# Performance work log

Measured on AMD Instinct MI355X. Metric: run time of the kernel, lower is better.

Reference implementation:

```python
import jax, jax.numpy as jnp
import numpy as np

B = 32768
N_TABLES = 26
N_ROWS = 200000
D = 64
N_DENSE = 13
NUM_PAIRS = (N_TABLES + 1) * N_TABLES // 2  # 351, pairs j < i over 27 vectors


def setup_inputs() -> dict:
    key = jax.random.key(0)
    ks = jax.random.split(key, 16)
    def lin(kw, kb, m, n):
        W = jax.random.normal(kw, (m, n), jnp.float32) * np.sqrt(2.0 / (m + n))
        b = jax.random.normal(kb, (m,), jnp.float32) * np.sqrt(1.0 / m)
        return W, b
    bw0, bb0 = lin(ks[0], ks[1], 512, N_DENSE)
    bw1, bb1 = lin(ks[2], ks[3], 256, 512)
    bw2, bb2 = lin(ks[4], ks[5], D, 256)
    tw0, tb0 = lin(ks[6], ks[7], 512, D + NUM_PAIRS)
    tw1, tb1 = lin(ks[8], ks[9], 256, 512)
    tw2, tb2 = lin(ks[10], ks[11], 1, 256)
    bound = np.sqrt(1.0 / N_ROWS)
    emb_tables = jax.random.uniform(ks[12], (N_TABLES, N_ROWS, D), jnp.float32,
                                    minval=-bound, maxval=bound)
    dense_x = jax.random.uniform(ks[13], (B, N_DENSE), jnp.float32)
    indices = jax.random.randint(ks[14], (N_TABLES, B), 0, N_ROWS, jnp.int64)
    return {"dense_x": dense_x, "indices": indices, "emb_tables": emb_tables,
            "bw0": bw0, "bb0": bb0, "bw1": bw1, "bb1": bb1, "bw2": bw2, "bb2": bb2,
            "tw0": tw0, "tb0": tb0, "tw1": tw1, "tb1": tb1, "tw2": tw2, "tb2": tb2}


def reference(dense_x, indices, emb_tables,
              bw0, bb0, bw1, bb1, bw2, bb2,
              tw0, tb0, tw1, tb1, tw2, tb2):
    # bottom MLP (all ReLU, sigmoid_bot = -1)
    h = jax.nn.relu(dense_x @ bw0.T + bb0)
    h = jax.nn.relu(h @ bw1.T + bb1)
    x_bot = jax.nn.relu(h @ bw2.T + bb2)          # [B, D]

    # multi-table EmbeddingBag(sum) with single-index bags -> plain gather
    embs = jax.vmap(lambda tbl, idx: tbl[idx])(emb_tables, indices)  # [26, B, D]

    # dot interaction over 27 feature vectors
    T = jnp.concatenate([x_bot[None], embs], axis=0).transpose(1, 0, 2)  # [B, 27, D]
    Z = jnp.einsum('bnd,bmd->bnm', T, T)                                 # [B, 27, 27]
    li, lj = jnp.tril_indices(N_TABLES + 1, k=-1)  # pairs with j < i (no self)
    Zflat = Z[:, li, lj]                           # [B, 351]
    R = jnp.concatenate([x_bot, Zflat], axis=1)    # [B, 415]

    # top MLP: ReLU, ReLU, Sigmoid (sigmoid_top = 2)
    h = jax.nn.relu(R @ tw0.T + tb0)
    h = jax.nn.relu(h @ tw1.T + tb1)
    p = jax.nn.sigmoid(h @ tw2.T + tb2)            # [B, 1]
    return p
```

## Files before the change

kernel.cpp:

```cpp
#include <hip/hip_runtime.h>
#include <cstddef>
#include <cstdint>

#define B_SZ    32768
#define NTAB    26
#define NROWS   200000

typedef __attribute__((ext_vector_type(8))) short short8v;
typedef __attribute__((ext_vector_type(4))) float f32x4;
typedef __attribute__((ext_vector_type(16))) float f32x16;

__device__ __forceinline__ ushort f2bf(float f) {
    uint32_t u = __builtin_bit_cast(uint32_t, f);
    u += 0x7FFFu + ((u >> 16) & 1u);
    return (ushort)(u >> 16);
}
__device__ __forceinline__ float bf2f(ushort h) {
    uint32_t u = ((uint32_t)h) << 16;
    return __builtin_bit_cast(float, u);
}
__device__ __forceinline__ void stage16(const ushort* g, ushort* l) {
    __builtin_amdgcn_global_load_lds(
        (const __attribute__((address_space(1))) unsigned int*)g,
        (__attribute__((address_space(3))) unsigned int*)l, 16, 0, 0);
}

__global__ __launch_bounds__(256) void conv_all_k(
    const float* __restrict__ dense_x, const float* __restrict__ bw0,
    const float* __restrict__ tw0, const float* __restrict__ bw1,
    const float* __restrict__ bw2, const float* __restrict__ tw1,
    ushort* __restrict__ dense_pad, ushort* __restrict__ bw0p,
    ushort* __restrict__ tw0p, ushort* __restrict__ bw1c,
    ushort* __restrict__ bw2c, ushort* __restrict__ tw1c)
{
    const int gid = blockIdx.x * 256 + threadIdx.x;
    if (gid < 1048576) {
        int r = gid >> 5, k = gid & 31;
        dense_pad[gid] = (k < 13) ? f2bf(dense_x[r * 13 + k]) : (ushort)0;
    } else if (gid < 1064960) {
        int i = gid - 1048576; int r = i >> 5, k = i & 31;
        bw0p[i] = (k < 13) ? f2bf(bw0[r * 13 + k]) : (ushort)0;
    } else if (gid < 1277952) {
        int i = gid - 1064960; int r = i / 416, k = i - r * 416;
        tw0p[i] = (k < 415) ? f2bf(tw0[r * 415 + k]) : (ushort)0;
    } else if (gid < 1409024) {
        int i = gid - 1277952; bw1c[i] = f2bf(bw1[i]);
    } else if (gid < 1425408) {
        int i = gid - 1409024; bw2c[i] = f2bf(bw2[i]);
    } else if (gid < 1556480) {
        int i = gid - 1425408; tw1c[i] = f2bf(tw1[i]);
    }
}

__global__ __launch_bounds__(256, 2) void bot012_k(
    const ushort* __restrict__ dense_pad, const ushort* __restrict__ bw0p,
    const float* __restrict__ bb0, const ushort* __restrict__ bw1c,
    const float* __restrict__ bb1, const ushort* __restrict__ bw2c,
    const float* __restrict__ bb2, ushort* __restrict__ Rb)
{
    __shared__ __align__(16) ushort h0s[32 * 512];
    __shared__ __align__(16) ushort Wst[2][256 * 32];
    __shared__ __align__(16) ushort h1s[32 * 256];
    const int t = threadIdx.x;
    const int lane = t & 63, w = t >> 6;
    const int fr = lane & 15, j16 = lane >> 4;
    const int bBase = blockIdx.x * 32;

    if (t < 128) {
        const int r = t >> 2, u = t & 3, us = u ^ ((r >> 1) & 3);
        stage16(dense_pad + (size_t)(bBase + r) * 32 + us * 8, &h1s[t * 8]);
    }
#pragma unroll
    for (int i = 0; i < 4; ++i) {
        const int idx = i * 256 + t;
        const int r = idx >> 2, u = idx & 3, us = u ^ ((r >> 1) & 3);
        stage16(bw0p + (size_t)r * 32 + us * 8, &Wst[0][idx * 8]);
        stage16(bw0p + (size_t)(256 + r) * 32 + us * 8, &Wst[1][idx * 8]);
    }
    __syncthreads();

    f32x4 acc0[2][2][4] = {};
    {
        short8v a[2];
#pragma unroll
        for (int m = 0; m < 2; ++m) {
            const int r = m * 16 + fr;
            a[m] = *(const short8v*)&h1s[r * 32 + (j16 ^ ((r >> 1) & 3)) * 8];
        }
#pragma unroll
        for (int hh = 0; hh < 2; ++hh) {
            short8v b[4];
#pragma unroll
            for (int n = 0; n < 4; ++n) {
                const int lr = w * 64 + n * 16 + fr;
                b[n] = *(const short8v*)&Wst[hh][lr * 32 + (j16 ^ ((lr >> 1) & 3)) * 8];
            }
            __builtin_amdgcn_s_setprio(1);
#pragma unroll
            for (int m = 0; m < 2; ++m)
#pragma unroll
                for (int n = 0; n < 4; ++n)
                    acc0[hh][m][n] = __builtin_amdgcn_mfma_f32_16x16x32_bf16(b[n], a[m], acc0[hh][m][n], 0, 0, 0);
            __builtin_amdgcn_s_setprio(0);
        }
    }
    __syncthreads();

#pragma unroll
    for (int i = 0; i < 4; ++i) {
        const int idx = i * 256 + t;
        const int r = idx >> 2, u = idx & 3, us = u ^ ((r >> 1) & 3);
        stage16(bw1c + (size_t)r * 512 + us * 8, &Wst[0][idx * 8]);
        stage16(bw1c + (size_t)r * 512 + 32 + us * 8, &Wst[1][idx * 8]);
    }
#pragma unroll
    for (int hh = 0; hh < 2; ++hh)
#pragma unroll
    for (int n = 0; n < 4; ++n) {
        const int ch = hh * 256 + w * 64 + n * 16 + j16 * 4;
        const float4 bv = *(const float4*)&bb0[ch];
#pragma unroll
        for (int m = 0; m < 2; ++m) {
            const int s = m * 16 + fr;
            ushort4 o;
            o.x = f2bf(fmaxf(acc0[hh][m][n][0] + bv.x, 0.f));
            o.y = f2bf(fmaxf(acc0[hh][m][n][1] + bv.y, 0.f));
            o.z = f2bf(fmaxf(acc0[hh][m][n][2] + bv.z, 0.f));
            o.w = f2bf(fmaxf(acc0[hh][m][n][3] + bv.w, 0.f));
            const int u = ch >> 3, su = u ^ (s & 7);
            *(ushort4*)&h0s[s * 512 + su * 8 + (ch & 7)] = o;
        }
    }
    __syncthreads();

    f32x4 acc1[2][4] = {};
    for (int i8 = 0; i8 < 8; ++i8) {
        const int ktA = i8 * 64, ktB = ktA + 32;
#pragma unroll
        for (int half = 0; half < 2; ++half) {
            const int kt = half ? ktB : ktA;
            short8v a[2], b[4];
#pragma unroll
            for (int m = 0; m < 2; ++m) {
                const int s = m * 16 + fr;
                const int u = (kt >> 3) + j16, su = u ^ (s & 7);
                a[m] = *(const short8v*)&h0s[s * 512 + su * 8];
            }
#pragma unroll
            for (int n = 0; n < 4; ++n) {
                const int lr = w * 64 + n * 16 + fr;
                b[n] = *(const short8v*)&Wst[half][lr * 32 + (j16 ^ ((lr >> 1) & 3)) * 8];
            }
            __builtin_amdgcn_s_setprio(1);
#pragma unroll
            for (int m = 0; m < 2; ++m)
#pragma unroll
                for (int n = 0; n < 4; ++n)
                    acc1[m][n] = __builtin_amdgcn_mfma_f32_16x16x32_bf16(b[n], a[m], acc1[m][n], 0, 0, 0);
            __builtin_amdgcn_s_setprio(0);
        }
        __syncthreads();
        if (i8 < 7) {
            const int kt2 = (i8 + 1) * 64;
#pragma unroll
            for (int i = 0; i < 4; ++i) {
                const int idx = i * 256 + t;
                const int r = idx >> 2, u = idx & 3, us = u ^ ((r >> 1) & 3);
                stage16(bw1c + (size_t)r * 512 + kt2 + us * 8, &Wst[0][idx * 8]);
                stage16(bw1c + (size_t)r * 512 + kt2 + 32 + us * 8, &Wst[1][idx * 8]);
            }
            __syncthreads();
        }
    }
    {
        const int r = t >> 2, u = t & 3, us = u ^ ((r >> 1) & 3);
        stage16(bw2c + (size_t)r * 256 + us * 8, &Wst[0][t * 8]);
        stage16(bw2c + (size_t)r * 256 + 32 + us * 8, &Wst[1][t * 8]);
    }
#pragma unroll
    for (int n = 0; n < 4; ++n) {
        const int ch = w * 64 + n * 16 + j16 * 4;
        const float4 bv = *(const float4*)&bb1[ch];
#pragma unroll
        for (int m = 0; m < 2; ++m) {
            const int s = m * 16 + fr;
            ushort4 o;
            o.x = f2bf(fmaxf(acc1[m][n][0] + bv.x, 0.f));
            o.y = f2bf(fmaxf(acc1[m][n][1] + bv.y, 0.f));
            o.z = f2bf(fmaxf(acc1[m][n][2] + bv.z, 0.f));
            o.w = f2bf(fmaxf(acc1[m][n][3] + bv.w, 0.f));
            const int u = ch >> 3, su = u ^ (s & 7);
            *(ushort4*)&h1s[s * 256 + su * 8 + (ch & 7)] = o;
        }
    }
    __syncthreads();

    f32x4 acc2[2] = {};
    for (int i8 = 0; i8 < 4; ++i8) {
#pragma unroll
        for (int half = 0; half < 2; ++half) {
            const int kt = i8 * 64 + half * 32;
            short8v a[2], b;
#pragma unroll
            for (int m = 0; m < 2; ++m) {
                const int s = m * 16 + fr;
                const int u = (kt >> 3) + j16, su = u ^ (s & 7);
                a[m] = *(const short8v*)&h1s[s * 256 + su * 8];
            }
            {
                const int lr = w * 16 + fr;
                b = *(const short8v*)&Wst[half][lr * 32 + (j16 ^ ((lr >> 1) & 3)) * 8];
            }
#pragma unroll
            for (int m = 0; m < 2; ++m)
                acc2[m] = __builtin_amdgcn_mfma_f32_16x16x32_bf16(b, a[m], acc2[m], 0, 0, 0);
        }
        __syncthreads();
        if (i8 < 3) {
            const int kt2 = (i8 + 1) * 64;
            const int r = t >> 2, u = t & 3, us = u ^ ((r >> 1) & 3);
            stage16(bw2c + (size_t)r * 256 + kt2 + us * 8, &Wst[0][t * 8]);
            stage16(bw2c + (size_t)r * 256 + kt2 + 32 + us * 8, &Wst[1][t * 8]);
            __syncthreads();
        }
    }
    {
        const int ch = w * 16 + j16 * 4;
        const float4 bv = *(const float4*)&bb2[ch];
#pragma unroll
        for (int m = 0; m < 2; ++m) {
            const int s = m * 16 + fr;
            ushort4 o;
            o.x = f2bf(fmaxf(acc2[m][0] + bv.x, 0.f));
            o.y = f2bf(fmaxf(acc2[m][1] + bv.y, 0.f));
            o.z = f2bf(fmaxf(acc2[m][2] + bv.z, 0.f));
            o.w = f2bf(fmaxf(acc2[m][3] + bv.w, 0.f));
            *(ushort4*)&Rb[(size_t)(bBase + s) * 64 + ch] = o;
        }
    }
}

__global__ __launch_bounds__(256, 2) void topint_k(
    const float* __restrict__ emb, const int* __restrict__ indices,
    const ushort* __restrict__ Rb, const ushort* __restrict__ tw0p,
    const float* __restrict__ tb0, const ushort* __restrict__ tw1c,
    const float* __restrict__ tb1, const float* __restrict__ tw2,
    const float* __restrict__ tb2, float* __restrict__ out)
{
    __shared__ __align__(16) ushort U[32 * 512];
    __shared__ __align__(16) ushort Wst[2][256 * 32];
    __shared__ __align__(16) int scratch[832];
    const int t = threadIdx.x;
    const int lane = t & 63, w = t >> 6;
    const int fr = lane & 15, j16 = lane >> 4;
    const int bBase = blockIdx.x * 32;

    {
        const int r = t >> 3, u = t & 7;
        short8v v = *(const short8v*)&Rb[(size_t)(bBase + r) * 64 + u * 8];
        *(short8v*)&U[r * 424 + u * 8] = v;
    }
    if (t < 32) U[t * 424 + 415] = 0;
    for (int e = t; e < 832; e += 256)
        scratch[e] = indices[(size_t)(e >> 5) * B_SZ + bBase + (e & 31)];
    __syncthreads();

#pragma unroll
    for (int i = 0; i < 4; ++i) {
        const int idx = i * 256 + t;
        const int r = idx >> 2, u = idx & 3, us = u ^ ((r >> 1) & 3);
        stage16(tw0p + (size_t)r * 416 + us * 8, &Wst[0][idx * 8]);
        stage16(tw0p + (size_t)(256 + r) * 416 + us * 8, &Wst[1][idx * 8]);
    }

    {
        const int r32 = lane & 31, half = lane >> 5;
        for (int it = 0; it < 8; ++it) {
            const int s = it * 4 + w;
            short8v tf[4];
            if (r32 == 0) {
#pragma unroll
                for (int kq = 0; kq < 4; ++kq)
                    tf[kq] = *(const short8v*)&U[s * 424 + kq * 16 + half * 8];
            } else if (r32 <= 26) {
                const int idxv = scratch[(r32 - 1) * 32 + s];
                const float* rp = emb + ((size_t)(r32 - 1) * NROWS + (size_t)idxv) * 64 + half * 8;
#pragma unroll
                for (int kq = 0; kq < 4; ++kq) {
                    const f32x4 x = *(const f32x4*)&rp[kq * 16];
                    const f32x4 y = *(const f32x4*)&rp[kq * 16 + 4];
                    short8v v;
                    v[0] = (short)f2bf(x[0]); v[1] = (short)f2bf(x[1]);
                    v[2] = (short)f2bf(x[2]); v[3] = (short)f2bf(x[3]);
                    v[4] = (short)f2bf(y[0]); v[5] = (short)f2bf(y[1]);
                    v[6] = (short)f2bf(y[2]); v[7] = (short)f2bf(y[3]);
                    tf[kq] = v;
                }
            } else {
#pragma unroll
                for (int kq = 0; kq < 4; ++kq) tf[kq] = (short8v)0;
            }
            f32x16 c = {};
#pragma unroll
            for (int kq = 0; kq < 4; ++kq)
                c = __builtin_amdgcn_mfma_f32_32x32x16_bf16(tf[kq], tf[kq], c, 0, 0, 0);
#pragma unroll
            for (int reg = 0; reg < 16; ++reg) {
                const int r = (reg & 3) + 8 * (reg >> 2) + 4 * half;
                if (r < 27 && r32 < r)
                    U[s * 424 + 64 + (r * (r - 1)) / 2 + r32] = f2bf(c[reg]);
            }
        }
    }
    __syncthreads();

    f32x4 accA[2][2][4] = {};
    for (int kt_i = 0; kt_i < 13; ++kt_i) {
        const int kt = kt_i * 32;
        short8v a[2];
#pragma unroll
        for (int m = 0; m < 2; ++m) {
            const int s = m * 16 + fr;
            a[m] = *(const short8v*)&U[s * 424 + ((kt >> 3) + j16) * 8];
        }
#pragma unroll
        for (int hh = 0; hh < 2; ++hh) {
            short8v b[4];
#pragma unroll
            for (int n = 0; n < 4; ++n) {
                const int lr = w * 64 + n * 16 + fr;
                b[n] = *(const short8v*)&Wst[hh][lr * 32 + (j16 ^ ((lr >> 1) & 3)) * 8];
            }
            __builtin_amdgcn_s_setprio(1);
#pragma unroll
            for (int m = 0; m < 2; ++m)
#pragma unroll
                for (int n = 0; n < 4; ++n)
                    accA[hh][m][n] = __builtin_amdgcn_mfma_f32_16x16x32_bf16(b[n], a[m], accA[hh][m][n], 0, 0, 0);
            __builtin_amdgcn_s_setprio(0);
        }
        __syncthreads();
        if (kt_i < 12) {
            const int kt2 = kt + 32;
#pragma unroll
            for (int i = 0; i < 4; ++i) {
                const int idx = i * 256 + t;
                const int r = idx >> 2, u = idx & 3, us = u ^ ((r >> 1) & 3);
                stage16(tw0p + (size_t)r * 416 + kt2 + us * 8, &Wst[0][idx * 8]);
                stage16(tw0p + (size_t)(256 + r) * 416 + kt2 + us * 8, &Wst[1][idx * 8]);
            }
            __syncthreads();
        }
    }
#pragma unroll
    for (int i = 0; i < 4; ++i) {
        const int idx = i * 256 + t;
        const int r = idx >> 2, u = idx & 3, us = u ^ ((r >> 1) & 3);
        stage16(tw1c + (size_t)r * 512 + us * 8, &Wst[0][idx * 8]);
        stage16(tw1c + (size_t)r * 512 + 32 + us * 8, &Wst[1][idx * 8]);
    }
#pragma unroll
    for (int hh = 0; hh < 2; ++hh)
#pragma unroll
    for (int n = 0; n < 4; ++n) {
        const int ch = hh * 256 + w * 64 + n * 16 + j16 * 4;
        const float4 bv = *(const float4*)&tb0[ch];
#pragma unroll
        for (int m = 0; m < 2; ++m) {
            const int s = m * 16 + fr;
            ushort4 o;
            o.x = f2bf(fmaxf(accA[hh][m][n][0] + bv.x, 0.f));
            o.y = f2bf(fmaxf(accA[hh][m][n][1] + bv.y, 0.f));
            o.z = f2bf(fmaxf(accA[hh][m][n][2] + bv.z, 0.f));
            o.w = f2bf(fmaxf(accA[hh][m][n][3] + bv.w, 0.f));
            const int u = ch >> 3, su = u ^ (s & 7);
            *(ushort4*)&U[s * 512 + su * 8 + (ch & 7)] = o;
        }
    }
    __syncthreads();

    f32x4 acc2[2][4] = {};
    for (int i8 = 0; i8 < 8; ++i8) {
#pragma unroll
        for (int half = 0; half < 2; ++half) {
            const int kt = i8 * 64 + half * 32;
            short8v a[2], b[4];
#pragma unroll
            for (int m = 0; m < 2; ++m) {
                const int s = m * 16 + fr;
                const int u = (kt >> 3) + j16, su = u ^ (s & 7);
                a[m] = *(const short8v*)&U[s * 512 + su * 8];
            }
#pragma unroll
            for (int n = 0; n < 4; ++n) {
                const int lr = w * 64 + n * 16 + fr;
                b[n] = *(const short8v*)&Wst[half][lr * 32 + (j16 ^ ((lr >> 1) & 3)) * 8];
            }
            __builtin_amdgcn_s_setprio(1);
#pragma unroll
            for (int m = 0; m < 2; ++m)
#pragma unroll
                for (int n = 0; n < 4; ++n)
                    acc2[m][n] = __builtin_amdgcn_mfma_f32_16x16x32_bf16(b[n], a[m], acc2[m][n], 0, 0, 0);
            __builtin_amdgcn_s_setprio(0);
        }
        __syncthreads();
        if (i8 < 7) {
            const int kt2 = (i8 + 1) * 64;
#pragma unroll
            for (int i = 0; i < 4; ++i) {
                const int idx = i * 256 + t;
                const int r = idx >> 2, u = idx & 3, us = u ^ ((r >> 1) & 3);
                stage16(tw1c + (size_t)r * 512 + kt2 + us * 8, &Wst[0][idx * 8]);
                stage16(tw1c + (size_t)r * 512 + kt2 + 32 + us * 8, &Wst[1][idx * 8]);
            }
            __syncthreads();
        }
    }

    float* red = (float*)scratch;
    float part[2] = {0.f, 0.f};
#pragma unroll
    for (int n = 0; n < 4; ++n) {
        const int ch = w * 64 + n * 16 + j16 * 4;
        const float4 bv = *(const float4*)&tb1[ch];
        const float4 wv = *(const float4*)&tw2[ch];
#pragma unroll
        for (int m = 0; m < 2; ++m) {
            part[m] += fmaxf(acc2[m][n][0] + bv.x, 0.f) * wv.x
                     + fmaxf(acc2[m][n][1] + bv.y, 0.f) * wv.y
                     + fmaxf(acc2[m][n][2] + bv.z, 0.f) * wv.z
                     + fmaxf(acc2[m][n][3] + bv.w, 0.f) * wv.w;
        }
    }
#pragma unroll
    for (int m = 0; m < 2; ++m) {
        float v = part[m];
        v += __shfl_xor(v, 16, 64);
        v += __shfl_xor(v, 32, 64);
        if (lane < 16) red[w * 32 + m * 16 + fr] = v;
    }
    __syncthreads();
    if (t < 32) {
        const float sm = red[t] + red[32 + t] + red[64 + t] + red[96 + t];
        out[bBase + t] = 1.f / (1.f + expf(-(sm + tb2[0])));
    }
}

extern "C" void kernel_launch(void* const* d_in, const int* in_sizes, int n_in,
                              void* d_out, int out_size, void* d_ws, size_t ws_size,
                              hipStream_t stream)
{
    (void)in_sizes; (void)n_in; (void)out_size; (void)ws_size;
    const float* dense_x = (const float*)d_in[0];
    const int*   indices = (const int*)d_in[1];
    const float* emb     = (const float*)d_in[2];
    const float* bw0 = (const float*)d_in[3];
    const float* bb0 = (const float*)d_in[4];
    const float* bw1 = (const float*)d_in[5];
    const float* bb1 = (const float*)d_in[6];
    const float* bw2 = (const float*)d_in[7];
    const float* bb2 = (const float*)d_in[8];
    const float* tw0 = (const float*)d_in[9];
    const float* tb0 = (const float*)d_in[10];
    const float* tw1 = (const float*)d_in[11];
    const float* tb1 = (const float*)d_in[12];
    const float* tw2 = (const float*)d_in[13];
    const float* tb2 = (const float*)d_in[14];
    float* out = (float*)d_out;

    ushort* ws16      = (ushort*)d_ws;
    ushort* dense_pad = ws16;
    ushort* Rb        = dense_pad + (size_t)B_SZ * 32;
    ushort* bw0p      = Rb + (size_t)B_SZ * 64;
    ushort* tw0p      = bw0p + 512 * 32;
    ushort* bw1c      = tw0p + 512 * 416;
    ushort* bw2c      = bw1c + 256 * 512;
    ushort* tw1c      = bw2c + 64 * 256;

    conv_all_k<<<dim3(6080), dim3(256), 0, stream>>>(
        dense_x, bw0, tw0, bw1, bw2, tw1,
        dense_pad, bw0p, tw0p, bw1c, bw2c, tw1c);

    bot012_k<<<dim3(B_SZ / 32), dim3(256), 0, stream>>>(
        dense_pad, bw0p, bb0, bw1c, bb1, bw2c, bb2, Rb);

    topint_k<<<dim3(B_SZ / 32), dim3(256), 0, stream>>>(
        emb, indices, Rb, tw0p, tb0, tw1c, tb1, tw2, tb2, out);
}
```

Measured before the change: 116.9 us.

## Fuse bottom MLP and interaction/top MLP into a single kernel

Merges the bottom-MLP kernel and the interaction+top-MLP kernel into one launch per 32-row tile. x_bot is written straight into the shared-memory R buffer instead of a global Rb round trip, and the shared buffers are reused across stages. The embedding indices are loaded into registers at kernel start so their latency overlaps with the bottom MLP. This removes one kernel launch and the global write/read of the intermediate, in exchange for longer register live ranges and a more complex single kernel.

```diff
diff --git a/kernel.cpp b/kernel.cpp
--- a/kernel.cpp
+++ b/kernel.cpp
@@ -14,10 +14,6 @@
     uint32_t u = __builtin_bit_cast(uint32_t, f);
     u += 0x7FFFu + ((u >> 16) & 1u);
     return (ushort)(u >> 16);
-}
-__device__ __forceinline__ float bf2f(ushort h) {
-    uint32_t u = ((uint32_t)h) << 16;
-    return __builtin_bit_cast(float, u);
 }
 __device__ __forceinline__ void stage16(const ushort* g, ushort* l) {
     __builtin_amdgcn_global_load_lds(
@@ -52,23 +48,34 @@
     }
 }
 
-__global__ __launch_bounds__(256, 2) void bot012_k(
+__global__ __launch_bounds__(256, 2) void fused_k(
     const ushort* __restrict__ dense_pad, const ushort* __restrict__ bw0p,
     const float* __restrict__ bb0, const ushort* __restrict__ bw1c,
     const float* __restrict__ bb1, const ushort* __restrict__ bw2c,
-    const float* __restrict__ bb2, ushort* __restrict__ Rb)
+    const float* __restrict__ bb2,
+    const float* __restrict__ emb, const int* __restrict__ indices,
+    const ushort* __restrict__ tw0p, const float* __restrict__ tb0,
+    const ushort* __restrict__ tw1c, const float* __restrict__ tb1,
+    const float* __restrict__ tw2, const float* __restrict__ tb2,
+    float* __restrict__ out)
 {
-    __shared__ __align__(16) ushort h0s[32 * 512];
+    __shared__ __align__(16) ushort R1[32 * 512];
     __shared__ __align__(16) ushort Wst[2][256 * 32];
-    __shared__ __align__(16) ushort h1s[32 * 256];
+    __shared__ __align__(16) ushort R3[32 * 256];
     const int t = threadIdx.x;
     const int lane = t & 63, w = t >> 6;
     const int fr = lane & 15, j16 = lane >> 4;
     const int bBase = blockIdx.x * 32;
 
+    int ir0, ir1, ir2, ir3;
+    ir0 = indices[(size_t)(t >> 5) * B_SZ + bBase + (t & 31)];
+    ir1 = indices[(size_t)((256 + t) >> 5) * B_SZ + bBase + ((256 + t) & 31)];
+    ir2 = indices[(size_t)((512 + t) >> 5) * B_SZ + bBase + ((512 + t) & 31)];
+    ir3 = (t < 64) ? indices[(size_t)((768 + t) >> 5) * B_SZ + bBase + ((768 + t) & 31)] : 0;
+
     if (t < 128) {
         const int r = t >> 2, u = t & 3, us = u ^ ((r >> 1) & 3);
-        stage16(dense_pad + (size_t)(bBase + r) * 32 + us * 8, &h1s[t * 8]);
+        stage16(dense_pad + (size_t)(bBase + r) * 32 + us * 8, &R3[t * 8]);
     }
 #pragma unroll
     for (int i = 0; i < 4; ++i) {
@@ -85,7 +92,7 @@
 #pragma unroll
         for (int m = 0; m < 2; ++m) {
             const int r = m * 16 + fr;
-            a[m] = *(const short8v*)&h1s[r * 32 + (j16 ^ ((r >> 1) & 3)) * 8];
+            a[m] = *(const short8v*)&R3[r * 32 + (j16 ^ ((r >> 1) & 3)) * 8];
         }
 #pragma unroll
         for (int hh = 0; hh < 2; ++hh) {
@@ -128,23 +135,22 @@
             o.z = f2bf(fmaxf(acc0[hh][m][n][2] + bv.z, 0.f));
             o.w = f2bf(fmaxf(acc0[hh][m][n][3] + bv.w, 0.f));
             const int u = ch >> 3, su = u ^ (s & 7);
-            *(ushort4*)&h0s[s * 512 + su * 8 + (ch & 7)] = o;
+            *(ushort4*)&R1[s * 512 + su * 8 + (ch & 7)] = o;
         }
     }
     __syncthreads();
 
     f32x4 acc1[2][4] = {};
     for (int i8 = 0; i8 < 8; ++i8) {
-        const int ktA = i8 * 64, ktB = ktA + 32;
 #pragma unroll
         for (int half = 0; half < 2; ++half) {
-            const int kt = half ? ktB : ktA;
+            const int kt = i8 * 64 + half * 32;
             short8v a[2], b[4];
 #pragma unroll
             for (int m = 0; m < 2; ++m) {
                 const int s = m * 16 + fr;
                 const int u = (kt >> 3) + j16, su = u ^ (s & 7);
-                a[m] = *(const short8v*)&h0s[s * 512 + su * 8];
+                a[m] = *(const short8v*)&R1[s * 512 + su * 8];
             }
 #pragma unroll
             for (int n = 0; n < 4; ++n) {
@@ -190,7 +196,7 @@
             o.z = f2bf(fmaxf(acc1[m][n][2] + bv.z, 0.f));
             o.w = f2bf(fmaxf(acc1[m][n][3] + bv.w, 0.f));
             const int u = ch >> 3, su = u ^ (s & 7);
-            *(ushort4*)&h1s[s * 256 + su * 8 + (ch & 7)] = o;
+            *(ushort4*)&R3[s * 256 + su * 8 + (ch & 7)] = o;
         }
     }
     __syncthreads();
@@ -205,7 +211,7 @@
             for (int m = 0; m < 2; ++m) {
                 const int s = m * 16 + fr;
                 const int u = (kt >> 3) + j16, su = u ^ (s & 7);
-                a[m] = *(const short8v*)&h1s[s * 256 + su * 8];
+                a[m] = *(const short8v*)&R3[s * 256 + su * 8];
             }
             {
                 const int lr = w * 16 + fr;
@@ -235,36 +241,15 @@
             o.y = f2bf(fmaxf(acc2[m][1] + bv.y, 0.f));
             o.z = f2bf(fmaxf(acc2[m][2] + bv.z, 0.f));
             o.w = f2bf(fmaxf(acc2[m][3] + bv.w, 0.f));
-            *(ushort4*)&Rb[(size_t)(bBase + s) * 64 + ch] = o;
-        }
-    }
-}
-
-__global__ __launch_bounds__(256, 2) void topint_k(
-    const float* __restrict__ emb, const int* __restrict__ indices,
-    const ushort* __restrict__ Rb, const ushort* __restrict__ tw0p,
-    const float* __restrict__ tb0, const ushort* __restrict__ tw1c,
-    const float* __restrict__ tb1, const float* __restrict__ tw2,
-    const float* __restrict__ tb2, float* __restrict__ out)
-{
-    __shared__ __align__(16) ushort U[32 * 512];
-    __shared__ __align__(16) ushort Wst[2][256 * 32];
-    __shared__ __align__(16) int scratch[832];
-    const int t = threadIdx.x;
-    const int lane = t & 63, w = t >> 6;
-    const int fr = lane & 15, j16 = lane >> 4;
-    const int bBase = blockIdx.x * 32;
-
+            *(ushort4*)&R1[s * 424 + ch] = o;
+        }
+    }
+    if (t < 32) R1[t * 424 + 415] = 0;
     {
-        const int r = t >> 3, u = t & 7;
-        short8v v = *(const short8v*)&Rb[(size_t)(bBase + r) * 64 + u * 8];
-        *(short8v*)&U[r * 424 + u * 8] = v;
-    }
-    if (t < 32) U[t * 424 + 415] = 0;
-    for (int e = t; e < 832; e += 256)
-        scratch[e] = indices[(size_t)(e >> 5) * B_SZ + bBase + (e & 31)];
-    __syncthreads();
-
+        int* sc = (int*)R3;
+        sc[t] = ir0; sc[256 + t] = ir1; sc[512 + t] = ir2;
+        if (t < 64) sc[768 + t] = ir3;
+    }
 #pragma unroll
     for (int i = 0; i < 4; ++i) {
         const int idx = i * 256 + t;
@@ -272,8 +257,10 @@
         stage16(tw0p + (size_t)r * 416 + us * 8, &Wst[0][idx * 8]);
         stage16(tw0p + (size_t)(256 + r) * 416 + us * 8, &Wst[1][idx * 8]);
     }
+    __syncthreads();
 
     {
+        const int* sc = (const int*)R3;
         const int r32 = lane & 31, half = lane >> 5;
         for (int it = 0; it < 8; ++it) {
             const int s = it * 4 + w;
@@ -281,9 +268,9 @@
             if (r32 == 0) {
 #pragma unroll
                 for (int kq = 0; kq < 4; ++kq)
-                    tf[kq] = *(const short8v*)&U[s * 424 + kq * 16 + half * 8];
+                    tf[kq] = *(const short8v*)&R1[s * 424 + kq * 16 + half * 8];
             } else if (r32 <= 26) {
-                const int idxv = scratch[(r32 - 1) * 32 + s];
+                const int idxv = sc[(r32 - 1) * 32 + s];
                 const float* rp = emb + ((size_t)(r32 - 1) * NROWS + (size_t)idxv) * 64 + half * 8;
 #pragma unroll
                 for (int kq = 0; kq < 4; ++kq) {
@@ -308,7 +295,7 @@
             for (int reg = 0; reg < 16; ++reg) {
                 const int r = (reg & 3) + 8 * (reg >> 2) + 4 * half;
                 if (r < 27 && r32 < r)
-                    U[s * 424 + 64 + (r * (r - 1)) / 2 + r32] = f2bf(c[reg]);
+                    R1[s * 424 + 64 + (r * (r - 1)) / 2 + r32] = f2bf(c[reg]);
             }
         }
     }
@@ -321,7 +308,7 @@
 #pragma unroll
         for (int m = 0; m < 2; ++m) {
             const int s = m * 16 + fr;
-            a[m] = *(const short8v*)&U[s * 424 + ((kt >> 3) + j16) * 8];
+            a[m] = *(const short8v*)&R1[s * 424 + ((kt >> 3) + j16) * 8];
         }
 #pragma unroll
         for (int hh = 0; hh < 2; ++hh) {
@@ -374,12 +361,12 @@
             o.z = f2bf(fmaxf(accA[hh][m][n][2] + bv.z, 0.f));
             o.w = f2bf(fmaxf(accA[hh][m][n][3] + bv.w, 0.f));
             const int u = ch >> 3, su = u ^ (s & 7);
-            *(ushort4*)&U[s * 512 + su * 8 + (ch & 7)] = o;
-        }
-    }
-    __syncthreads();
-
-    f32x4 acc2[2][4] = {};
+            *(ushort4*)&R1[s * 512 + su * 8 + (ch & 7)] = o;
+        }
+    }
+    __syncthreads();
+
+    f32x4 accB[2][4] = {};
     for (int i8 = 0; i8 < 8; ++i8) {
 #pragma unroll
         for (int half = 0; half < 2; ++half) {
@@ -389,7 +376,7 @@
             for (int m = 0; m < 2; ++m) {
                 const int s = m * 16 + fr;
                 const int u = (kt >> 3) + j16, su = u ^ (s & 7);
-                a[m] = *(const short8v*)&U[s * 512 + su * 8];
+                a[m] = *(const short8v*)&R1[s * 512 + su * 8];
             }
 #pragma unroll
             for (int n = 0; n < 4; ++n) {
@@ -401,7 +388,7 @@
             for (int m = 0; m < 2; ++m)
 #pragma unroll
                 for (int n = 0; n < 4; ++n)
-                    acc2[m][n] = __builtin_amdgcn_mfma_f32_16x16x32_bf16(b[n], a[m], acc2[m][n], 0, 0, 0);
+                    accB[m][n] = __builtin_amdgcn_mfma_f32_16x16x32_bf16(b[n], a[m], accB[m][n], 0, 0, 0);
             __builtin_amdgcn_s_setprio(0);
         }
         __syncthreads();
@@ -418,7 +405,7 @@
         }
     }
 
-    float* red = (float*)scratch;
+    float* red = (float*)R3;
     float part[2] = {0.f, 0.f};
 #pragma unroll
     for (int n = 0; n < 4; ++n) {
@@ -427,10 +414,10 @@
         const float4 wv = *(const float4*)&tw2[ch];
 #pragma unroll
         for (int m = 0; m < 2; ++m) {
-            part[m] += fmaxf(acc2[m][n][0] + bv.x, 0.f) * wv.x
-                     + fmaxf(acc2[m][n][1] + bv.y, 0.f) * wv.y
-                     + fmaxf(acc2[m][n][2] + bv.z, 0.f) * wv.z
-                     + fmaxf(acc2[m][n][3] + bv.w, 0.f) * wv.w;
+            part[m] += fmaxf(accB[m][n][0] + bv.x, 0.f) * wv.x
+                     + fmaxf(accB[m][n][1] + bv.y, 0.f) * wv.y
+                     + fmaxf(accB[m][n][2] + bv.z, 0.f) * wv.z
+                     + fmaxf(accB[m][n][3] + bv.w, 0.f) * wv.w;
         }
     }
 #pragma unroll
@@ -471,8 +458,7 @@
 
     ushort* ws16      = (ushort*)d_ws;
     ushort* dense_pad = ws16;
-    ushort* Rb        = dense_pad + (size_t)B_SZ * 32;
-    ushort* bw0p      = Rb + (size_t)B_SZ * 64;
+    ushort* bw0p      = dense_pad + (size_t)B_SZ * 32;
     ushort* tw0p      = bw0p + 512 * 32;
     ushort* bw1c      = tw0p + 512 * 416;
     ushort* bw2c      = bw1c + 256 * 512;
@@ -482,9 +468,7 @@
         dense_x, bw0, tw0, bw1, bw2, tw1,
         dense_pad, bw0p, tw0p, bw1c, bw2c, tw1c);
 
-    bot012_k<<<dim3(B_SZ / 32), dim3(256), 0, stream>>>(
-        dense_pad, bw0p, bb0, bw1c, bb1, bw2c, bb2, Rb);
-
-    topint_k<<<dim3(B_SZ / 32), dim3(256), 0, stream>>>(
-        emb, indices, Rb, tw0p, tb0, tw1c, tb1, tw2, tb2, out);
+    fused_k<<<dim3(B_SZ / 32), dim3(256), 0, stream>>>(
+        dense_pad, bw0p, bb0, bw1c, bb1, bw2c, bb2,
+        emb, indices, tw0p, tb0, tw1c, tb1, tw2, tb2, out);
 }
```

Measured after the change: 112.2 us. 1.04x faster.
